# Kernel optimization log

Hardware: AMD Instinct MI355X
Metric: run time of the kernel (lower is better)

## Reference

```python
import jax, jax.numpy as jnp
import numpy as np

POOL = 7
STRIDE = 16.0


def setup_inputs() -> dict:
    key = jax.random.key(0)
    k1, k2, k3, k4, k5 = jax.random.split(key, 5)
    image = jax.random.normal(k1, (1, 128, 128, 512), dtype=jnp.float32)
    N = 1000
    # RoIs in input-image pixel coords: (x_center, y_center, w, h)
    w = jax.random.uniform(k2, (N,), minval=32.0, maxval=480.0)
    h = jax.random.uniform(k3, (N,), minval=32.0, maxval=480.0)
    x0 = jax.random.uniform(k4, (N,), minval=0.0, maxval=1500.0)
    y0 = jax.random.uniform(k5, (N,), minval=0.0, maxval=1500.0)
    RoI = jnp.stack([x0 + w / 2, y0 + h / 2, w, h], axis=1).astype(jnp.float32)
    return {"image": image, "RoI_inImage": RoI}


def _axis_coords(start, size, pool, limit):
    """Half-pixel bilinear sample coords for resizing a [size]-long crop
    starting at `start` to `pool` samples (matches tf.image.resize bilinear).
    Returns (i0, i1, frac) each [N, pool]."""
    grid = (jnp.arange(pool, dtype=jnp.float32) + 0.5) / pool  # [pool]
    s = grid[None, :] * size[:, None] - 0.5                    # crop-relative
    s = jnp.clip(s, 0.0, size[:, None] - 1.0)
    f0 = jnp.floor(s)
    frac = s - f0
    f1 = jnp.minimum(f0 + 1.0, size[:, None] - 1.0)
    i0 = jnp.clip(start[:, None] + f0, 0, limit - 1).astype(jnp.int32)
    i1 = jnp.clip(start[:, None] + f1, 0, limit - 1).astype(jnp.int32)
    return i0, i1, frac


def _roi_pool(image, RoI):
    H, W = image.shape[1], image.shape[2]
    feat = image[0]  # [H, W, C]
    x, y, w, h = RoI[:, 0], RoI[:, 1], RoI[:, 2], RoI[:, 3]
    # integer crop bounds on the stride-16 feature map (non-differentiable)
    r = jax.lax.stop_gradient(jnp.round((x - w / 2) / STRIDE))   # col start
    c = jax.lax.stop_gradient(jnp.round((y - h / 2) / STRIDE))   # row start
    wq = jax.lax.stop_gradient(jnp.maximum(jnp.round(w / STRIDE), 1.0))
    hq = jax.lax.stop_gradient(jnp.maximum(jnp.round(h / STRIDE), 1.0))
    iy0, iy1, ly = _axis_coords(c, hq, POOL, H)  # rows   [N, P]
    ix0, ix1, lx = _axis_coords(r, wq, POOL, W)  # cols   [N, P]
    # gather 4 corners: [N, P, P, C]
    g = lambda iy, ix: feat[iy[:, :, None], ix[:, None, :]]
    ly_ = ly[:, :, None, None]
    lx_ = lx[:, None, :, None]
    out = ((1 - ly_) * (1 - lx_) * g(iy0, ix0)
           + (1 - ly_) * lx_ * g(iy0, ix1)
           + ly_ * (1 - lx_) * g(iy1, ix0)
           + ly_ * lx_ * g(iy1, ix1))
    N = RoI.shape[0]
    return out.reshape(1, N, POOL, POOL, feat.shape[-1])


def reference(image, RoI_inImage):
    return _roi_pool(image, RoI_inImage)
```

## Files before the change

### kernel.cpp

```cpp
#include <hip/hip_runtime.h>

#define POOL   7
#define RSTRIDE 16.0f
#define IMG_H  128
#define IMG_W  128
#define IMG_C  512

__global__ __launch_bounds__(128)
void RoiPoolingLayer_22462678958491_kernel(const float* __restrict__ image,
                                           const float* __restrict__ roi,
                                           float* __restrict__ out)
{
    const int b   = blockIdx.x;
    const int n   = b / (POOL * POOL);
    const int rem = b - n * (POOL * POOL);
    const int py  = rem / POOL;
    const int px  = rem - py * POOL;

    const float x = roi[n * 4 + 0];
    const float y = roi[n * 4 + 1];
    const float w = roi[n * 4 + 2];
    const float h = roi[n * 4 + 3];

    const float r  = rintf((x - 0.5f * w) / RSTRIDE);
    const float c  = rintf((y - 0.5f * h) / RSTRIDE);
    const float wq = fmaxf(rintf(w / RSTRIDE), 1.0f);
    const float hq = fmaxf(rintf(h / RSTRIDE), 1.0f);

    float sy = (((float)py + 0.5f) / (float)POOL) * hq - 0.5f;
    sy = fminf(fmaxf(sy, 0.0f), hq - 1.0f);
    const float fy0 = floorf(sy);
    const float ly  = sy - fy0;
    const float fy1 = fminf(fy0 + 1.0f, hq - 1.0f);
    const int iy0 = (int)fminf(fmaxf(c + fy0, 0.0f), (float)(IMG_H - 1));
    const int iy1 = (int)fminf(fmaxf(c + fy1, 0.0f), (float)(IMG_H - 1));

    float sx = (((float)px + 0.5f) / (float)POOL) * wq - 0.5f;
    sx = fminf(fmaxf(sx, 0.0f), wq - 1.0f);
    const float fx0 = floorf(sx);
    const float lx  = sx - fx0;
    const float fx1 = fminf(fx0 + 1.0f, wq - 1.0f);
    const int ix0 = (int)fminf(fmaxf(r + fx0, 0.0f), (float)(IMG_W - 1));
    const int ix1 = (int)fminf(fmaxf(r + fx1, 0.0f), (float)(IMG_W - 1));

    const float w00 = (1.0f - ly) * (1.0f - lx);
    const float w01 = (1.0f - ly) * lx;
    const float w10 = ly * (1.0f - lx);
    const float w11 = ly * lx;

    const float4* p00 = (const float4*)(image + ((size_t)iy0 * IMG_W + ix0) * IMG_C);
    const float4* p01 = (const float4*)(image + ((size_t)iy0 * IMG_W + ix1) * IMG_C);
    const float4* p10 = (const float4*)(image + ((size_t)iy1 * IMG_W + ix0) * IMG_C);
    const float4* p11 = (const float4*)(image + ((size_t)iy1 * IMG_W + ix1) * IMG_C);
    float4*       po  = (float4*)(out + (size_t)b * IMG_C);

    const int t = threadIdx.x;
    const float4 a  = p00[t];
    const float4 bb = p01[t];
    const float4 cc = p10[t];
    const float4 dd = p11[t];

    float4 o;
    o.x = w00 * a.x + w01 * bb.x + w10 * cc.x + w11 * dd.x;
    o.y = w00 * a.y + w01 * bb.y + w10 * cc.y + w11 * dd.y;
    o.z = w00 * a.z + w01 * bb.z + w10 * cc.z + w11 * dd.z;
    o.w = w00 * a.w + w01 * bb.w + w10 * cc.w + w11 * dd.w;
    po[t] = o;
}

extern "C" void kernel_launch(void* const* d_in, const int* in_sizes, int n_in,
                              void* d_out, int out_size, void* d_ws, size_t ws_size,
                              hipStream_t stream)
{
    const float* image = (const float*)d_in[0];
    const float* roi   = (const float*)d_in[1];
    float*       out   = (float*)d_out;

    const int N = in_sizes[1] / 4;
    const int blocks = N * POOL * POOL;

    RoiPoolingLayer_22462678958491_kernel<<<blocks, 128, 0, stream>>>(image, roi, out);
}
```

Baseline: 156.9 us.

## Process a full pooled row per block and swizzle RoIs across XCDs

Each block now handles one RoI output row, looping over all 7 pooled columns instead of one output cell. This cuts the block count sevenfold and shares the RoI and row-coordinate setup across columns. A block-index swizzle gives each XCD a contiguous range of RoIs, so neighbouring rows of the same RoI hit the same L2. In exchange there is less parallelism per launch, and loads inside each block are serialised through the unrolled loop.

```diff
diff --git a/kernel.cpp b/kernel.cpp
--- a/kernel.cpp
+++ b/kernel.cpp
@@ -1,21 +1,30 @@
 #include <hip/hip_runtime.h>
 
-#define POOL   7
+#define POOL    7
 #define RSTRIDE 16.0f
-#define IMG_H  128
-#define IMG_W  128
-#define IMG_C  512
+#define IMG_H   128
+#define IMG_W   128
+#define IMG_C   512
+#define C4      (IMG_C / 4)
 
+template <bool SWIZZLE>
 __global__ __launch_bounds__(128)
 void RoiPoolingLayer_22462678958491_kernel(const float* __restrict__ image,
                                            const float* __restrict__ roi,
-                                           float* __restrict__ out)
+                                           float* __restrict__ out, int N)
 {
-    const int b   = blockIdx.x;
-    const int n   = b / (POOL * POOL);
-    const int rem = b - n * (POOL * POOL);
-    const int py  = rem / POOL;
-    const int px  = rem - py * POOL;
+    int n, py;
+    if (SWIZZLE) {
+        const int per   = N >> 3;
+        const int xcd   = blockIdx.x & 7;
+        const int local = blockIdx.x >> 3;
+        const int q     = local / POOL;
+        n  = xcd * per + q;
+        py = local - q * POOL;
+    } else {
+        n  = blockIdx.x / POOL;
+        py = blockIdx.x - n * POOL;
+    }
 
     const float x = roi[n * 4 + 0];
     const float y = roi[n * 4 + 1];
@@ -35,37 +44,38 @@
     const int iy0 = (int)fminf(fmaxf(c + fy0, 0.0f), (float)(IMG_H - 1));
     const int iy1 = (int)fminf(fmaxf(c + fy1, 0.0f), (float)(IMG_H - 1));
 
-    float sx = (((float)px + 0.5f) / (float)POOL) * wq - 0.5f;
-    sx = fminf(fmaxf(sx, 0.0f), wq - 1.0f);
-    const float fx0 = floorf(sx);
-    const float lx  = sx - fx0;
-    const float fx1 = fminf(fx0 + 1.0f, wq - 1.0f);
-    const int ix0 = (int)fminf(fmaxf(r + fx0, 0.0f), (float)(IMG_W - 1));
-    const int ix1 = (int)fminf(fmaxf(r + fx1, 0.0f), (float)(IMG_W - 1));
+    const int t = threadIdx.x;
+    const float4* row0 = (const float4*)(image + (size_t)iy0 * IMG_W * IMG_C) + t;
+    const float4* row1 = (const float4*)(image + (size_t)iy1 * IMG_W * IMG_C) + t;
+    float4* po = (float4*)(out + ((size_t)n * (POOL * POOL) + (size_t)py * POOL) * IMG_C) + t;
 
-    const float w00 = (1.0f - ly) * (1.0f - lx);
-    const float w01 = (1.0f - ly) * lx;
-    const float w10 = ly * (1.0f - lx);
-    const float w11 = ly * lx;
+#pragma unroll
+    for (int px = 0; px < POOL; ++px) {
+        float sx = (((float)px + 0.5f) / (float)POOL) * wq - 0.5f;
+        sx = fminf(fmaxf(sx, 0.0f), wq - 1.0f);
+        const float fx0 = floorf(sx);
+        const float lx  = sx - fx0;
+        const float fx1 = fminf(fx0 + 1.0f, wq - 1.0f);
+        const int ix0 = (int)fminf(fmaxf(r + fx0, 0.0f), (float)(IMG_W - 1));
+        const int ix1 = (int)fminf(fmaxf(r + fx1, 0.0f), (float)(IMG_W - 1));
 
-    const float4* p00 = (const float4*)(image + ((size_t)iy0 * IMG_W + ix0) * IMG_C);
-    const float4* p01 = (const float4*)(image + ((size_t)iy0 * IMG_W + ix1) * IMG_C);
-    const float4* p10 = (const float4*)(image + ((size_t)iy1 * IMG_W + ix0) * IMG_C);
-    const float4* p11 = (const float4*)(image + ((size_t)iy1 * IMG_W + ix1) * IMG_C);
-    float4*       po  = (float4*)(out + (size_t)b * IMG_C);
+        const float w00 = (1.0f - ly) * (1.0f - lx);
+        const float w01 = (1.0f - ly) * lx;
+        const float w10 = ly * (1.0f - lx);
+        const float w11 = ly * lx;
 
-    const int t = threadIdx.x;
-    const float4 a  = p00[t];
-    const float4 bb = p01[t];
-    const float4 cc = p10[t];
-    const float4 dd = p11[t];
+        const float4 a  = row0[ix0 * C4];
+        const float4 bb = row0[ix1 * C4];
+        const float4 cc = row1[ix0 * C4];
+        const float4 dd = row1[ix1 * C4];
 
-    float4 o;
-    o.x = w00 * a.x + w01 * bb.x + w10 * cc.x + w11 * dd.x;
-    o.y = w00 * a.y + w01 * bb.y + w10 * cc.y + w11 * dd.y;
-    o.z = w00 * a.z + w01 * bb.z + w10 * cc.z + w11 * dd.z;
-    o.w = w00 * a.w + w01 * bb.w + w10 * cc.w + w11 * dd.w;
-    po[t] = o;
+        float4 o;
+        o.x = w00 * a.x + w01 * bb.x + w10 * cc.x + w11 * dd.x;
+        o.y = w00 * a.y + w01 * bb.y + w10 * cc.y + w11 * dd.y;
+        o.z = w00 * a.z + w01 * bb.z + w10 * cc.z + w11 * dd.z;
+        o.w = w00 * a.w + w01 * bb.w + w10 * cc.w + w11 * dd.w;
+        po[px * C4] = o;
+    }
 }
 
 extern "C" void kernel_launch(void* const* d_in, const int* in_sizes, int n_in,
@@ -77,7 +87,11 @@
     float*       out   = (float*)d_out;
 
     const int N = in_sizes[1] / 4;
-    const int blocks = N * POOL * POOL;
+    const int blocks = N * POOL;
 
-    RoiPoolingLayer_22462678958491_kernel<<<blocks, 128, 0, stream>>>(image, roi, out);
+    if ((N & 7) == 0) {
+        RoiPoolingLayer_22462678958491_kernel<true><<<blocks, 128, 0, stream>>>(image, roi, out, N);
+    } else {
+        RoiPoolingLayer_22462678958491_kernel<false><<<blocks, 128, 0, stream>>>(image, roi, out, N);
+    }
 }
```

Result: faster. 150.1 us (-4.4%).
